# Optimization experiments

Measured on AMD Instinct MI355X. Metric: run time of the kernel, lower is better.

The kernel has to match this reference:

```python
import jax, jax.numpy as jnp
import numpy as np

N_NODES = 100000
N_EDGES = 800000
D_IN = 256
D_HID = 256
D_OUT = 64


def _gcn_conv(x, W, b, src, dst, deg_inv_sqrt, n_nodes):
    """PyG GCNConv: out = D^{-1/2}(A+I)D^{-1/2} (x @ W) + b.
    src/dst already include self-loops; deg_inv_sqrt precomputed over them."""
    h = x @ W  # [N, Dh]
    norm = deg_inv_sqrt[src] * deg_inv_sqrt[dst]  # [E+N]
    msg = h[src] * norm[:, None]  # gather + scale, [E+N, Dh]
    out = jax.ops.segment_sum(msg, dst, num_segments=n_nodes)  # scatter-add
    return out + b


def setup_inputs() -> dict:
    key = jax.random.key(0)
    ks = jax.random.split(key, 8)
    x = jax.random.normal(ks[0], (N_NODES, D_IN), jnp.float32)
    edge_index = jax.random.randint(ks[1], (2, N_EDGES), 0, N_NODES, dtype=jnp.int32)
    W1 = jax.random.normal(ks[2], (D_IN, D_HID), jnp.float32) * (1.0 / np.sqrt(D_IN))
    b1 = jnp.zeros((D_HID,), jnp.float32)
    W2 = jax.random.normal(ks[3], (D_HID, D_HID), jnp.float32) * (1.0 / np.sqrt(D_HID))
    b2 = jnp.zeros((D_HID,), jnp.float32)
    Wo = jax.random.normal(ks[4], (D_HID, D_OUT), jnp.float32) * (1.0 / np.sqrt(D_HID))
    bo = jnp.zeros((D_OUT,), jnp.float32)
    return {"x": x, "edge_index": edge_index, "W1": W1, "b1": b1,
            "W2": W2, "b2": b2, "Wo": Wo, "bo": bo}


def reference(x, edge_index, W1, b1, W2, b2, Wo, bo):
    n = x.shape[0]
    loops = jnp.arange(n, dtype=edge_index.dtype)
    src = jnp.concatenate([edge_index[0], loops])  # add self-loops
    dst = jnp.concatenate([edge_index[1], loops])
    # degree over target nodes (incl. self-loops), symmetric normalization
    deg = jax.ops.segment_sum(jnp.ones(dst.shape[0], x.dtype), dst, num_segments=n)
    deg_inv_sqrt = jax.lax.rsqrt(deg)  # deg >= 1 thanks to self-loops

    h = _gcn_conv(x, W1, b1, src, dst, deg_inv_sqrt, n)
    h = jax.nn.relu(h)
    # dropout p=0.0 -> identity
    h = _gcn_conv(h, W2, b2, src, dst, deg_inv_sqrt, n)
    h = jax.nn.relu(h)
    logits = h @ Wo + bo
    return jax.nn.log_softmax(logits, axis=1)
```

## Files before the change

kernel.cpp:

```cpp
#include <hip/hip_runtime.h>
#include <math.h>

#define TPB 256

typedef short bf16x8 __attribute__((ext_vector_type(8)));
typedef unsigned short u16x8 __attribute__((ext_vector_type(8)));
typedef float f32x4 __attribute__((ext_vector_type(4)));

__device__ __forceinline__ float bf2f(unsigned short u) {
  union { unsigned int i; float f; } c;
  c.i = ((unsigned int)u) << 16;
  return c.f;
}
__device__ __forceinline__ unsigned short f2bf(float f) {
  union { float f; unsigned int i; } c;
  c.f = f;
  unsigned int r = c.i + 0x7FFFu + ((c.i >> 16) & 1u);
  return (unsigned short)(r >> 16);
}


__global__ __launch_bounds__(TPB) void zero_cnt_k(int* __restrict__ cnt, int N) {
  int i = blockIdx.x * TPB + threadIdx.x;
  if (i < N) cnt[i] = 0;
}

__global__ __launch_bounds__(TPB) void count_k(const int* __restrict__ dstv,
                                               int* __restrict__ cnt, int E) {
  int e = blockIdx.x * TPB + threadIdx.x;
  if (e < E) atomicAdd(&cnt[dstv[e]], 1);
}

__global__ __launch_bounds__(TPB) void scan1_k(const int* __restrict__ cnt,
                                               int* __restrict__ excl,
                                               int* __restrict__ blk_sums, int N) {
  __shared__ int sh[TPB];
  int b = blockIdx.x, tid = threadIdx.x;
  int base = b * 1024 + tid * 4;
  int v[4];
  int sum = 0;
#pragma unroll
  for (int j = 0; j < 4; ++j) {
    int i = base + j;
    v[j] = (i < N) ? cnt[i] : 0;
    sum += v[j];
  }
  sh[tid] = sum;
  __syncthreads();
  for (int off = 1; off < TPB; off <<= 1) {
    int t = (tid >= off) ? sh[tid - off] : 0;
    __syncthreads();
    sh[tid] += t;
    __syncthreads();
  }
  if (tid == TPB - 1) blk_sums[b] = sh[TPB - 1];
  int run = (tid > 0) ? sh[tid - 1] : 0;
#pragma unroll
  for (int j = 0; j < 4; ++j) {
    int i = base + j;
    if (i < N) excl[i] = run;
    run += v[j];
  }
}

__global__ __launch_bounds__(TPB) void scan2_k(int* __restrict__ blk_sums, int NB) {
  __shared__ int sh[TPB];
  int tid = threadIdx.x;
  sh[tid] = (tid < NB) ? blk_sums[tid] : 0;
  __syncthreads();
  for (int off = 1; off < TPB; off <<= 1) {
    int t = (tid >= off) ? sh[tid - off] : 0;
    __syncthreads();
    sh[tid] += t;
    __syncthreads();
  }
  int ex = (tid > 0) ? sh[tid - 1] : 0;
  if (tid < NB) blk_sums[tid] = ex;
}

__global__ __launch_bounds__(TPB) void finalize_k(int* __restrict__ row_ptr,
                                                  const int* __restrict__ blk_sums,
                                                  int* __restrict__ cursor,
                                                  const int* __restrict__ cnt,
                                                  float* __restrict__ dis, int N, int E) {
  int i = blockIdx.x * TPB + threadIdx.x;
  if (i < N) {
    int r = row_ptr[i] + blk_sums[i >> 10];
    row_ptr[i] = r;
    cursor[i] = r;
    dis[i] = rsqrtf((float)(cnt[i] + 1));
  }
  if (blockIdx.x == 0 && threadIdx.x == 0) row_ptr[N] = E;
}

__global__ __launch_bounds__(TPB) void fill_k(const int* __restrict__ srcv,
                                              const int* __restrict__ dstv,
                                              int* __restrict__ cursor,
                                              int* __restrict__ col_src, int E) {
  int e = blockIdx.x * TPB + threadIdx.x;
  if (e < E) {
    int d = dstv[e];
    int pos = atomicAdd(&cursor[d], 1);
    col_src[pos] = srcv[e];
  }
}


__global__ __launch_bounds__(TPB) void cvt_bf16_k(const float* __restrict__ in,
                                                  unsigned short* __restrict__ out,
                                                  long n) {
  long i = ((long)blockIdx.x * TPB + threadIdx.x) * 8;
  if (i >= n) return;
  float4 a = *(const float4*)(in + i);
  float4 b = *(const float4*)(in + i + 4);
  ushort4 o0, o1;
  o0.x = f2bf(a.x); o0.y = f2bf(a.y); o0.z = f2bf(a.z); o0.w = f2bf(a.w);
  o1.x = f2bf(b.x); o1.y = f2bf(b.y); o1.z = f2bf(b.z); o1.w = f2bf(b.w);
  *(ushort4*)(out + i) = o0;
  *(ushort4*)(out + i + 4) = o1;
}

__global__ __launch_bounds__(TPB) void wt_k(const float* __restrict__ W,
                                            unsigned short* __restrict__ Wt) {
  int idx = blockIdx.x * TPB + threadIdx.x;
  int n = idx >> 8, k = idx & 255;
  Wt[n * 256 + k] = f2bf(W[k * 256 + n]);
}


__global__ __launch_bounds__(TPB) void gemm_bf16_k(const unsigned short* __restrict__ A,
                                                   const unsigned short* __restrict__ Bt,
                                                   unsigned short* __restrict__ C,
                                                   int M) {
  __shared__ unsigned short As[128 * 32];
  __shared__ unsigned short Bs[128 * 32];
  const int tid = threadIdx.x;
  const int m0 = blockIdx.y * 128;
  const int n0 = blockIdx.x * 128;
  const int lane = tid & 63;
  const int wid = tid >> 6;
  const int wr = (wid >> 1) * 64;
  const int wc = (wid & 1) * 64;

  const int srow = tid >> 1;
  const int scb0 = (tid & 1) * 2;
  const int grow = min(m0 + srow, M - 1);
  const unsigned short* gA = A + (size_t)grow * 256 + scb0 * 8;
  const unsigned short* gB = Bt + (size_t)(n0 + srow) * 256 + scb0 * 8;
  const int swz = (srow >> 1) & 3;
  const int ls0 = srow * 64 + ((scb0 ^ swz) << 4);
  const int ls1 = srow * 64 + (((scb0 + 1) ^ swz) << 4);

  const int r15 = lane & 15;
  const int cq = lane >> 4;
  const int swzr = (r15 >> 1) & 3;
  const int coff = ((cq ^ swzr) << 4);

  f32x4 acc[4][4];
#pragma unroll
  for (int i = 0; i < 4; ++i)
#pragma unroll
    for (int j = 0; j < 4; ++j)
#pragma unroll
      for (int r = 0; r < 4; ++r) acc[i][j][r] = 0.f;

  u16x8 ra0 = *(const u16x8*)(gA);
  u16x8 ra1 = *(const u16x8*)(gA + 8);
  u16x8 rb0 = *(const u16x8*)(gB);
  u16x8 rb1 = *(const u16x8*)(gB + 8);

  for (int kt = 0; kt < 8; ++kt) {
    __syncthreads();
    *(u16x8*)((char*)As + ls0) = ra0;
    *(u16x8*)((char*)As + ls1) = ra1;
    *(u16x8*)((char*)Bs + ls0) = rb0;
    *(u16x8*)((char*)Bs + ls1) = rb1;
    __syncthreads();
    if (kt < 7) {
      ra0 = *(const u16x8*)(gA + (kt + 1) * 32);
      ra1 = *(const u16x8*)(gA + (kt + 1) * 32 + 8);
      rb0 = *(const u16x8*)(gB + (kt + 1) * 32);
      rb1 = *(const u16x8*)(gB + (kt + 1) * 32 + 8);
    }
    bf16x8 af[4], bfr[4];
#pragma unroll
    for (int i = 0; i < 4; ++i)
      af[i] = *(const bf16x8*)((char*)As + (wr + i * 16 + r15) * 64 + coff);
#pragma unroll
    for (int j = 0; j < 4; ++j)
      bfr[j] = *(const bf16x8*)((char*)Bs + (wc + j * 16 + r15) * 64 + coff);
#pragma unroll
    for (int i = 0; i < 4; ++i)
#pragma unroll
      for (int j = 0; j < 4; ++j)
        acc[i][j] = __builtin_amdgcn_mfma_f32_16x16x32_bf16(af[i], bfr[j], acc[i][j], 0, 0, 0);
  }

#pragma unroll
  for (int i = 0; i < 4; ++i) {
#pragma unroll
    for (int r = 0; r < 4; ++r) {
      int row = m0 + wr + i * 16 + (lane >> 4) * 4 + r;
      if (row < M) {
#pragma unroll
        for (int j = 0; j < 4; ++j) {
          C[(size_t)row * 256 + n0 + wc + j * 16 + r15] = f2bf(acc[i][j][r]);
        }
      }
    }
  }
}


__global__ __launch_bounds__(TPB) void aggregate_bf_k(const unsigned short* __restrict__ H,
                                                      unsigned short* __restrict__ O,
                                                      const int* __restrict__ row_ptr,
                                                      const int* __restrict__ col_src,
                                                      const float* __restrict__ dis,
                                                      const float* __restrict__ bias,
                                                      int N) {
  int wid = (blockIdx.x * TPB + threadIdx.x) >> 6;
  int lane = threadIdx.x & 63;
  if (wid >= N) return;
  int beg = row_ptr[wid], end = row_ptr[wid + 1];
  float a0 = 0.f, a1 = 0.f, a2 = 0.f, a3 = 0.f;
  for (int e = beg; e < end; ++e) {
    int s = col_src[e];
    float w = dis[s];
    ushort4 h = *(const ushort4*)(H + (size_t)s * 256 + lane * 4);
    a0 = fmaf(w, bf2f(h.x), a0);
    a1 = fmaf(w, bf2f(h.y), a1);
    a2 = fmaf(w, bf2f(h.z), a2);
    a3 = fmaf(w, bf2f(h.w), a3);
  }
  float dv = dis[wid];
  float dv2 = dv * dv;
  ushort4 hv = *(const ushort4*)(H + (size_t)wid * 256 + lane * 4);
  float4 b = *(const float4*)(bias + lane * 4);
  ushort4 o;
  o.x = f2bf(fmaxf(fmaf(dv, a0, fmaf(dv2, bf2f(hv.x), b.x)), 0.f));
  o.y = f2bf(fmaxf(fmaf(dv, a1, fmaf(dv2, bf2f(hv.y), b.y)), 0.f));
  o.z = f2bf(fmaxf(fmaf(dv, a2, fmaf(dv2, bf2f(hv.z), b.z)), 0.f));
  o.w = f2bf(fmaxf(fmaf(dv, a3, fmaf(dv2, bf2f(hv.w), b.w)), 0.f));
  *(ushort4*)(O + (size_t)wid * 256 + lane * 4) = o;
}


#define OBM 128
#define OBK 16
#define OLDA 132
#define OLDB 72
#define OLDL 65

__global__ __launch_bounds__(TPB) void outgemm_k(const unsigned short* __restrict__ H,
                                                 const float* __restrict__ Wo,
                                                 const float* __restrict__ bo,
                                                 float* __restrict__ out, int M) {
  __shared__ float As[OBK][OLDA];
  __shared__ float Bs[OBK][OLDB];
  __shared__ float Ls[OBM][OLDL];
  int tid = threadIdx.x;
  int tx = tid & 7;
  int ty = tid >> 3;
  int m0 = blockIdx.x * OBM;

  float4 bi0 = *(const float4*)(bo + tx * 8);
  float4 bi1 = *(const float4*)(bo + tx * 8 + 4);
  float acc[4][8];
#pragma unroll
  for (int i = 0; i < 4; ++i) {
    acc[i][0] = bi0.x; acc[i][1] = bi0.y; acc[i][2] = bi0.z; acc[i][3] = bi0.w;
    acc[i][4] = bi1.x; acc[i][5] = bi1.y; acc[i][6] = bi1.z; acc[i][7] = bi1.w;
  }

  int ar = tid >> 1;
  int akh = (tid & 1) * 8;
  int br = tid >> 4;
  int bc4 = (tid & 15) * 4;

  for (int k0 = 0; k0 < 256; k0 += OBK) {
    {
      int gr = m0 + ar;
      if (gr < M) {
        u16x8 v = *(const u16x8*)(H + (size_t)gr * 256 + k0 + akh);
        As[akh + 0][ar] = bf2f(v[0]);
        As[akh + 1][ar] = bf2f(v[1]);
        As[akh + 2][ar] = bf2f(v[2]);
        As[akh + 3][ar] = bf2f(v[3]);
        As[akh + 4][ar] = bf2f(v[4]);
        As[akh + 5][ar] = bf2f(v[5]);
        As[akh + 6][ar] = bf2f(v[6]);
        As[akh + 7][ar] = bf2f(v[7]);
      } else {
#pragma unroll
        for (int j = 0; j < 8; ++j) As[akh + j][ar] = 0.f;
      }
    }
    *(float4*)&Bs[br][bc4] = *(const float4*)(Wo + (size_t)(k0 + br) * 64 + bc4);
    __syncthreads();
#pragma unroll
    for (int kk = 0; kk < OBK; ++kk) {
      float4 a = *(const float4*)&As[kk][ty * 4];
      float4 b0 = *(const float4*)&Bs[kk][tx * 8];
      float4 b1 = *(const float4*)&Bs[kk][tx * 8 + 4];
      float av[4] = {a.x, a.y, a.z, a.w};
      float bv[8] = {b0.x, b0.y, b0.z, b0.w, b1.x, b1.y, b1.z, b1.w};
#pragma unroll
      for (int i = 0; i < 4; ++i)
#pragma unroll
        for (int j = 0; j < 8; ++j) acc[i][j] = fmaf(av[i], bv[j], acc[i][j]);
    }
    __syncthreads();
  }

#pragma unroll
  for (int i = 0; i < 4; ++i) {
    int r = ty * 4 + i;
    *(float4*)&Ls[r][tx * 8] = make_float4(acc[i][0], acc[i][1], acc[i][2], acc[i][3]);
    *(float4*)&Ls[r][tx * 8 + 4] = make_float4(acc[i][4], acc[i][5], acc[i][6], acc[i][7]);
  }
  __syncthreads();

  int lane = tid & 63;
  int w = tid >> 6;
  for (int r = w * 32; r < w * 32 + 32; ++r) {
    int grow = m0 + r;
    if (grow >= M) break;
    float v = Ls[r][lane];
    float mx = v;
    for (int o = 32; o > 0; o >>= 1) mx = fmaxf(mx, __shfl_xor(mx, o, 64));
    float ex = expf(v - mx);
    float s = ex;
    for (int o = 32; o > 0; o >>= 1) s += __shfl_xor(s, o, 64);
    out[(size_t)grow * 64 + lane] = (v - mx) - logf(s);
  }
}


extern "C" void kernel_launch(void* const* d_in, const int* in_sizes, int n_in,
                              void* d_out, int out_size, void* d_ws, size_t ws_size,
                              hipStream_t stream) {
  const float* x = (const float*)d_in[0];
  const int* ei = (const int*)d_in[1];
  const float* W1 = (const float*)d_in[2];
  const float* b1 = (const float*)d_in[3];
  const float* W2 = (const float*)d_in[4];
  const float* b2 = (const float*)d_in[5];
  const float* Wo = (const float*)d_in[6];
  const float* bo = (const float*)d_in[7];
  float* out = (float*)d_out;

  const int Dh = 256;
  const int N = in_sizes[0] / Dh;
  const int E = in_sizes[1] / 2;
  const int* srcv = ei;
  const int* dstv = ei + E;

  char* p = (char*)d_ws;
  auto take = [&](size_t bytes) {
    char* r = p;
    p += (bytes + 255) & ~(size_t)255;
    return r;
  };
  unsigned short* xbf = (unsigned short*)take((size_t)N * Dh * 2);
  unsigned short* hbuf1 = (unsigned short*)take((size_t)N * Dh * 2);
  unsigned short* hbuf2 = (unsigned short*)take((size_t)N * Dh * 2);
  unsigned short* Wt1 = (unsigned short*)take(256 * 256 * 2);
  unsigned short* Wt2 = (unsigned short*)take(256 * 256 * 2);
  float* dis = (float*)take((size_t)N * 4);
  int* cnt = (int*)take((size_t)N * 4);
  int* row_ptr = (int*)take((size_t)(N + 1) * 4);
  int* cursor = (int*)take((size_t)N * 4);
  int* col_src = (int*)take((size_t)E * 4);
  int* blk_sums = (int*)take(4096 * 4);

  int NB = (N + 1023) / 1024;

  long nx = (long)N * Dh;
  cvt_bf16_k<<<(int)((nx / 8 + TPB - 1) / TPB), TPB, 0, stream>>>(x, xbf, nx);
  wt_k<<<256, TPB, 0, stream>>>(W1, Wt1);
  wt_k<<<256, TPB, 0, stream>>>(W2, Wt2);
  zero_cnt_k<<<(N + TPB - 1) / TPB, TPB, 0, stream>>>(cnt, N);
  count_k<<<(E + TPB - 1) / TPB, TPB, 0, stream>>>(dstv, cnt, E);
  scan1_k<<<NB, TPB, 0, stream>>>(cnt, row_ptr, blk_sums, N);
  scan2_k<<<1, TPB, 0, stream>>>(blk_sums, NB);
  finalize_k<<<(N + TPB - 1) / TPB, TPB, 0, stream>>>(row_ptr, blk_sums, cursor, cnt, dis, N, E);
  fill_k<<<(E + TPB - 1) / TPB, TPB, 0, stream>>>(srcv, dstv, cursor, col_src, E);

  dim3 ggrid(2, (N + 127) / 128);

  gemm_bf16_k<<<ggrid, TPB, 0, stream>>>(xbf, Wt1, hbuf1, N);
  aggregate_bf_k<<<(N + 3) / 4, TPB, 0, stream>>>(hbuf1, hbuf2, row_ptr, col_src, dis, b1, N);
  gemm_bf16_k<<<ggrid, TPB, 0, stream>>>(hbuf2, Wt2, hbuf1, N);
  aggregate_bf_k<<<(N + 3) / 4, TPB, 0, stream>>>(hbuf1, hbuf2, row_ptr, col_src, dis, b2, N);
  outgemm_k<<<(N + OBM - 1) / OBM, TPB, 0, stream>>>(hbuf2, Wo, bo, out, N);
}
```

Before: 621.6 us.

## Prescale GEMM rows by deg^-1/2, unroll aggregation, move output GEMM to MFMA

The source-side normalization is folded into the epilogue of the hidden GEMM, so each row is multiplied by dis[row]. This removes the per-edge dis[s] gather and the multiply in aggregation. The aggregation loop is unrolled by four with independent accumulators so more gathers are in flight at once. The output GEMM is rewritten to use bf16 MFMA with a pre-transposed bf16 Wo instead of fp32 FMA in shared memory, which adds one more bf16 rounding of Wo.

```diff
diff --git a/kernel.cpp b/kernel.cpp
--- a/kernel.cpp
+++ b/kernel.cpp
@@ -127,10 +127,18 @@
   Wt[n * 256 + k] = f2bf(W[k * 256 + n]);
 }
 
+__global__ __launch_bounds__(TPB) void wot_k(const float* __restrict__ Wo,
+                                             unsigned short* __restrict__ Wot) {
+  int idx = blockIdx.x * TPB + threadIdx.x;
+  int n = idx >> 8, k = idx & 255;
+  Wot[n * 256 + k] = f2bf(Wo[k * 64 + n]);
+}
+
 
 __global__ __launch_bounds__(TPB) void gemm_bf16_k(const unsigned short* __restrict__ A,
                                                    const unsigned short* __restrict__ Bt,
                                                    unsigned short* __restrict__ C,
+                                                   const float* __restrict__ dis,
                                                    int M) {
   __shared__ unsigned short As[128 * 32];
   __shared__ unsigned short Bs[128 * 32];
@@ -202,9 +210,10 @@
     for (int r = 0; r < 4; ++r) {
       int row = m0 + wr + i * 16 + (lane >> 4) * 4 + r;
       if (row < M) {
+        float dv = dis[row];
 #pragma unroll
         for (int j = 0; j < 4; ++j) {
-          C[(size_t)row * 256 + n0 + wc + j * 16 + r15] = f2bf(acc[i][j][r]);
+          C[(size_t)row * 256 + n0 + wc + j * 16 + r15] = f2bf(dv * acc[i][j][r]);
         }
       }
     }
@@ -223,116 +232,144 @@
   int lane = threadIdx.x & 63;
   if (wid >= N) return;
   int beg = row_ptr[wid], end = row_ptr[wid + 1];
-  float a0 = 0.f, a1 = 0.f, a2 = 0.f, a3 = 0.f;
-  for (int e = beg; e < end; ++e) {
+
+  float p0 = 0.f, p1 = 0.f, p2 = 0.f, p3 = 0.f;
+  float q0 = 0.f, q1 = 0.f, q2 = 0.f, q3 = 0.f;
+  float r0 = 0.f, r1 = 0.f, r2 = 0.f, r3 = 0.f;
+  float t0 = 0.f, t1 = 0.f, t2 = 0.f, t3 = 0.f;
+
+  int e = beg;
+  for (; e + 4 <= end; e += 4) {
+    int s0 = col_src[e + 0];
+    int s1 = col_src[e + 1];
+    int s2 = col_src[e + 2];
+    int s3 = col_src[e + 3];
+    ushort4 h0 = *(const ushort4*)(H + (size_t)s0 * 256 + lane * 4);
+    ushort4 h1 = *(const ushort4*)(H + (size_t)s1 * 256 + lane * 4);
+    ushort4 h2 = *(const ushort4*)(H + (size_t)s2 * 256 + lane * 4);
+    ushort4 h3 = *(const ushort4*)(H + (size_t)s3 * 256 + lane * 4);
+    p0 += bf2f(h0.x); p1 += bf2f(h0.y); p2 += bf2f(h0.z); p3 += bf2f(h0.w);
+    q0 += bf2f(h1.x); q1 += bf2f(h1.y); q2 += bf2f(h1.z); q3 += bf2f(h1.w);
+    r0 += bf2f(h2.x); r1 += bf2f(h2.y); r2 += bf2f(h2.z); r3 += bf2f(h2.w);
+    t0 += bf2f(h3.x); t1 += bf2f(h3.y); t2 += bf2f(h3.z); t3 += bf2f(h3.w);
+  }
+  for (; e < end; ++e) {
     int s = col_src[e];
-    float w = dis[s];
     ushort4 h = *(const ushort4*)(H + (size_t)s * 256 + lane * 4);
-    a0 = fmaf(w, bf2f(h.x), a0);
-    a1 = fmaf(w, bf2f(h.y), a1);
-    a2 = fmaf(w, bf2f(h.z), a2);
-    a3 = fmaf(w, bf2f(h.w), a3);
-  }
+    p0 += bf2f(h.x); p1 += bf2f(h.y); p2 += bf2f(h.z); p3 += bf2f(h.w);
+  }
+
+  ushort4 hv = *(const ushort4*)(H + (size_t)wid * 256 + lane * 4);
+  p0 += bf2f(hv.x); p1 += bf2f(hv.y); p2 += bf2f(hv.z); p3 += bf2f(hv.w);
+
+  float s0 = (p0 + q0) + (r0 + t0);
+  float s1 = (p1 + q1) + (r1 + t1);
+  float s2 = (p2 + q2) + (r2 + t2);
+  float s3 = (p3 + q3) + (r3 + t3);
+
   float dv = dis[wid];
-  float dv2 = dv * dv;
-  ushort4 hv = *(const ushort4*)(H + (size_t)wid * 256 + lane * 4);
   float4 b = *(const float4*)(bias + lane * 4);
   ushort4 o;
-  o.x = f2bf(fmaxf(fmaf(dv, a0, fmaf(dv2, bf2f(hv.x), b.x)), 0.f));
-  o.y = f2bf(fmaxf(fmaf(dv, a1, fmaf(dv2, bf2f(hv.y), b.y)), 0.f));
-  o.z = f2bf(fmaxf(fmaf(dv, a2, fmaf(dv2, bf2f(hv.z), b.z)), 0.f));
-  o.w = f2bf(fmaxf(fmaf(dv, a3, fmaf(dv2, bf2f(hv.w), b.w)), 0.f));
+  o.x = f2bf(fmaxf(fmaf(dv, s0, b.x), 0.f));
+  o.y = f2bf(fmaxf(fmaf(dv, s1, b.y), 0.f));
+  o.z = f2bf(fmaxf(fmaf(dv, s2, b.z), 0.f));
+  o.w = f2bf(fmaxf(fmaf(dv, s3, b.w), 0.f));
   *(ushort4*)(O + (size_t)wid * 256 + lane * 4) = o;
 }
 
 
-#define OBM 128
-#define OBK 16
-#define OLDA 132
-#define OLDB 72
-#define OLDL 65
-
 __global__ __launch_bounds__(TPB) void outgemm_k(const unsigned short* __restrict__ H,
-                                                 const float* __restrict__ Wo,
+                                                 const unsigned short* __restrict__ Wot,
                                                  const float* __restrict__ bo,
                                                  float* __restrict__ out, int M) {
-  __shared__ float As[OBK][OLDA];
-  __shared__ float Bs[OBK][OLDB];
-  __shared__ float Ls[OBM][OLDL];
-  int tid = threadIdx.x;
-  int tx = tid & 7;
-  int ty = tid >> 3;
-  int m0 = blockIdx.x * OBM;
-
-  float4 bi0 = *(const float4*)(bo + tx * 8);
-  float4 bi1 = *(const float4*)(bo + tx * 8 + 4);
-  float acc[4][8];
-#pragma unroll
-  for (int i = 0; i < 4; ++i) {
-    acc[i][0] = bi0.x; acc[i][1] = bi0.y; acc[i][2] = bi0.z; acc[i][3] = bi0.w;
-    acc[i][4] = bi1.x; acc[i][5] = bi1.y; acc[i][6] = bi1.z; acc[i][7] = bi1.w;
-  }
-
-  int ar = tid >> 1;
-  int akh = (tid & 1) * 8;
-  int br = tid >> 4;
-  int bc4 = (tid & 15) * 4;
-
-  for (int k0 = 0; k0 < 256; k0 += OBK) {
-    {
-      int gr = m0 + ar;
-      if (gr < M) {
-        u16x8 v = *(const u16x8*)(H + (size_t)gr * 256 + k0 + akh);
-        As[akh + 0][ar] = bf2f(v[0]);
-        As[akh + 1][ar] = bf2f(v[1]);
-        As[akh + 2][ar] = bf2f(v[2]);
-        As[akh + 3][ar] = bf2f(v[3]);
-        As[akh + 4][ar] = bf2f(v[4]);
-        As[akh + 5][ar] = bf2f(v[5]);
-        As[akh + 6][ar] = bf2f(v[6]);
-        As[akh + 7][ar] = bf2f(v[7]);
-      } else {
-#pragma unroll
-        for (int j = 0; j < 8; ++j) As[akh + j][ar] = 0.f;
+  __shared__ unsigned short As[128 * 32];
+  __shared__ unsigned short Bs[64 * 32];
+  __shared__ float Ls[128][65];
+  const int tid = threadIdx.x;
+  const int m0 = blockIdx.x * 128;
+  const int lane = tid & 63;
+  const int w = tid >> 6;
+  const int wr = w * 32;
+
+  const int srow = tid >> 1;
+  const int scb0 = (tid & 1) * 2;
+  const int grow = min(m0 + srow, M - 1);
+  const unsigned short* gA = H + (size_t)grow * 256 + scb0 * 8;
+  const int swz = (srow >> 1) & 3;
+  const int lsa0 = srow * 64 + ((scb0 ^ swz) << 4);
+  const int lsa1 = srow * 64 + (((scb0 + 1) ^ swz) << 4);
+
+  const int brow = tid >> 2;
+  const int bcb = tid & 3;
+  const unsigned short* gB = Wot + (size_t)brow * 256 + bcb * 8;
+  const int bswz = (brow >> 1) & 3;
+  const int lsb = brow * 64 + ((bcb ^ bswz) << 4);
+
+  const int r15 = lane & 15;
+  const int cq = lane >> 4;
+  const int swzr = (r15 >> 1) & 3;
+  const int coff = ((cq ^ swzr) << 4);
+
+  f32x4 acc[2][4];
+#pragma unroll
+  for (int i = 0; i < 2; ++i)
+#pragma unroll
+    for (int j = 0; j < 4; ++j)
+#pragma unroll
+      for (int r = 0; r < 4; ++r) acc[i][j][r] = 0.f;
+
+  u16x8 ra0 = *(const u16x8*)(gA);
+  u16x8 ra1 = *(const u16x8*)(gA + 8);
+  u16x8 rb = *(const u16x8*)(gB);
+
+  for (int kt = 0; kt < 8; ++kt) {
+    __syncthreads();
+    *(u16x8*)((char*)As + lsa0) = ra0;
+    *(u16x8*)((char*)As + lsa1) = ra1;
+    *(u16x8*)((char*)Bs + lsb) = rb;
+    __syncthreads();
+    if (kt < 7) {
+      ra0 = *(const u16x8*)(gA + (kt + 1) * 32);
+      ra1 = *(const u16x8*)(gA + (kt + 1) * 32 + 8);
+      rb = *(const u16x8*)(gB + (kt + 1) * 32);
+    }
+    bf16x8 af[2], bfr[4];
+#pragma unroll
+    for (int i = 0; i < 2; ++i)
+      af[i] = *(const bf16x8*)((char*)As + (wr + i * 16 + r15) * 64 + coff);
+#pragma unroll
+    for (int j = 0; j < 4; ++j)
+      bfr[j] = *(const bf16x8*)((char*)Bs + (j * 16 + r15) * 64 + coff);
+#pragma unroll
+    for (int i = 0; i < 2; ++i)
+#pragma unroll
+      for (int j = 0; j < 4; ++j)
+        acc[i][j] = __builtin_amdgcn_mfma_f32_16x16x32_bf16(af[i], bfr[j], acc[i][j], 0, 0, 0);
+  }
+
+#pragma unroll
+  for (int j = 0; j < 4; ++j) {
+    float bj = bo[j * 16 + r15];
+#pragma unroll
+    for (int i = 0; i < 2; ++i)
+#pragma unroll
+      for (int r = 0; r < 4; ++r) {
+        int rl = wr + i * 16 + (lane >> 4) * 4 + r;
+        Ls[rl][j * 16 + r15] = acc[i][j][r] + bj;
       }
-    }
-    *(float4*)&Bs[br][bc4] = *(const float4*)(Wo + (size_t)(k0 + br) * 64 + bc4);
-    __syncthreads();
-#pragma unroll
-    for (int kk = 0; kk < OBK; ++kk) {
-      float4 a = *(const float4*)&As[kk][ty * 4];
-      float4 b0 = *(const float4*)&Bs[kk][tx * 8];
-      float4 b1 = *(const float4*)&Bs[kk][tx * 8 + 4];
-      float av[4] = {a.x, a.y, a.z, a.w};
-      float bv[8] = {b0.x, b0.y, b0.z, b0.w, b1.x, b1.y, b1.z, b1.w};
-#pragma unroll
-      for (int i = 0; i < 4; ++i)
-#pragma unroll
-        for (int j = 0; j < 8; ++j) acc[i][j] = fmaf(av[i], bv[j], acc[i][j]);
-    }
-    __syncthreads();
-  }
-
-#pragma unroll
-  for (int i = 0; i < 4; ++i) {
-    int r = ty * 4 + i;
-    *(float4*)&Ls[r][tx * 8] = make_float4(acc[i][0], acc[i][1], acc[i][2], acc[i][3]);
-    *(float4*)&Ls[r][tx * 8 + 4] = make_float4(acc[i][4], acc[i][5], acc[i][6], acc[i][7]);
   }
   __syncthreads();
 
-  int lane = tid & 63;
-  int w = tid >> 6;
-  for (int r = w * 32; r < w * 32 + 32; ++r) {
-    int grow = m0 + r;
-    if (grow >= M) break;
+  for (int r = wr; r < wr + 32; ++r) {
+    int gr = m0 + r;
+    if (gr >= M) break;
     float v = Ls[r][lane];
     float mx = v;
     for (int o = 32; o > 0; o >>= 1) mx = fmaxf(mx, __shfl_xor(mx, o, 64));
     float ex = expf(v - mx);
     float s = ex;
     for (int o = 32; o > 0; o >>= 1) s += __shfl_xor(s, o, 64);
-    out[(size_t)grow * 64 + lane] = (v - mx) - logf(s);
+    out[(size_t)gr * 64 + lane] = (v - mx) - logf(s);
   }
 }
 
@@ -367,6 +404,7 @@
   unsigned short* hbuf2 = (unsigned short*)take((size_t)N * Dh * 2);
   unsigned short* Wt1 = (unsigned short*)take(256 * 256 * 2);
   unsigned short* Wt2 = (unsigned short*)take(256 * 256 * 2);
+  unsigned short* Wot = (unsigned short*)take(64 * 256 * 2);
   float* dis = (float*)take((size_t)N * 4);
   int* cnt = (int*)take((size_t)N * 4);
   int* row_ptr = (int*)take((size_t)(N + 1) * 4);
@@ -380,6 +418,7 @@
   cvt_bf16_k<<<(int)((nx / 8 + TPB - 1) / TPB), TPB, 0, stream>>>(x, xbf, nx);
   wt_k<<<256, TPB, 0, stream>>>(W1, Wt1);
   wt_k<<<256, TPB, 0, stream>>>(W2, Wt2);
+  wot_k<<<64, TPB, 0, stream>>>(Wo, Wot);
   zero_cnt_k<<<(N + TPB - 1) / TPB, TPB, 0, stream>>>(cnt, N);
   count_k<<<(E + TPB - 1) / TPB, TPB, 0, stream>>>(dstv, cnt, E);
   scan1_k<<<NB, TPB, 0, stream>>>(cnt, row_ptr, blk_sums, N);
@@ -389,9 +428,9 @@
 
   dim3 ggrid(2, (N + 127) / 128);
 
-  gemm_bf16_k<<<ggrid, TPB, 0, stream>>>(xbf, Wt1, hbuf1, N);
+  gemm_bf16_k<<<ggrid, TPB, 0, stream>>>(xbf, Wt1, hbuf1, dis, N);
   aggregate_bf_k<<<(N + 3) / 4, TPB, 0, stream>>>(hbuf1, hbuf2, row_ptr, col_src, dis, b1, N);
-  gemm_bf16_k<<<ggrid, TPB, 0, stream>>>(hbuf2, Wt2, hbuf1, N);
+  gemm_bf16_k<<<ggrid, TPB, 0, stream>>>(hbuf2, Wt2, hbuf1, dis, N);
   aggregate_bf_k<<<(N + 3) / 4, TPB, 0, stream>>>(hbuf1, hbuf2, row_ptr, col_src, dis, b2, N);
-  outgemm_k<<<(N + OBM - 1) / OBM, TPB, 0, stream>>>(hbuf2, Wo, bo, out, N);
-}
+  outgemm_k<<<(N + 127) / 128, TPB, 0, stream>>>(hbuf2, Wot, bo, out, N);
+}
```

New measurement: 530.0 us. 14.7% less time.
